# Optimization experiments

Hardware: AMD Instinct MI355X
Metric: run time of the kernel (lower is better)

The kernel has to match this reference:

```python
import jax, jax.numpy as jnp
import numpy as np

D = 256
H = 8
HD = D // H
LN_EPS = 1e-5


def setup_inputs() -> dict:
    key = jax.random.key(0)
    ks = jax.random.split(key, 20)
    N = 768
    s = lambda *sh: 1.0 / np.sqrt(sh[-1])
    inp = {
        "features": jax.random.normal(ks[0], (N, D), jnp.float32),
        "boxes": jax.random.uniform(ks[1], (N, 4), jnp.float32),
        # MultiheadAttention params (torch layout: [out, in])
        "in_proj_w": jax.random.normal(ks[2], (3 * D, D), jnp.float32) * s(D),
        "in_proj_b": jnp.zeros((3 * D,), jnp.float32),
        "out_proj_w": jax.random.normal(ks[3], (D, D), jnp.float32) * s(D),
        "out_proj_b": jnp.zeros((D,), jnp.float32),
        # similarity_net params
        "w1": jax.random.normal(ks[4], (256, 3 * D + 3), jnp.float32) * s(3 * D + 3),
        "b1": jnp.zeros((256,), jnp.float32),
        "ln_g": jnp.ones((256,), jnp.float32),
        "ln_b": jnp.zeros((256,), jnp.float32),
        "w2": jax.random.normal(ks[5], (128, 256), jnp.float32) * s(256),
        "b2": jnp.zeros((128,), jnp.float32),
        "w3": jax.random.normal(ks[6], (64, 128), jnp.float32) * s(128),
        "b3": jnp.zeros((64,), jnp.float32),
        "w4": jax.random.normal(ks[7], (32, 64), jnp.float32) * s(64),
        "b4": jnp.zeros((32,), jnp.float32),
        "w5": jax.random.normal(ks[8], (1, 32), jnp.float32) * s(32),
        "b5": jnp.zeros((1,), jnp.float32),
    }
    return inp


def _mha(x, in_w, in_b, out_w, out_b):
    # x: [N, D]; torch nn.MultiheadAttention self-attention (eval mode)
    N = x.shape[0]
    qkv = x @ in_w.T + in_b                      # [N, 3D]
    q, k, v = jnp.split(qkv, 3, axis=-1)
    q = q.reshape(N, H, HD).transpose(1, 0, 2)   # [H, N, HD]
    k = k.reshape(N, H, HD).transpose(1, 0, 2)
    v = v.reshape(N, H, HD).transpose(1, 0, 2)
    scores = jnp.einsum("hnd,hmd->hnm", q, k) / np.sqrt(HD)
    attn = jax.nn.softmax(scores, axis=-1)
    o = jnp.einsum("hnm,hmd->hnd", attn, v)      # [H, N, HD]
    o = o.transpose(1, 0, 2).reshape(N, D)
    return o @ out_w.T + out_b


def reference(features, boxes, in_proj_w, in_proj_b, out_proj_w, out_proj_b,
              w1, b1, ln_g, ln_b, w2, b2, w3, b3, w4, b4, w5, b5):
    N = features.shape[0]
    att = _mha(features, in_proj_w, in_proj_b, out_proj_w, out_proj_b)  # [N, D]

    fi = jnp.broadcast_to(att[:, None, :], (N, N, D))
    fj = jnp.broadcast_to(att[None, :, :], (N, N, D))
    bi = boxes[:, None, :]
    bj = boxes[None, :, :]
    x_dist = jnp.abs(bi[:, :, 0] - bj[:, :, 0])
    y_diff = bi[:, :, 1] - bj[:, :, 1]
    spatial = jnp.stack([x_dist, jnp.abs(y_diff), y_diff], axis=-1)    # [N, N, 3]
    pairs = jnp.concatenate([fi, fj, fi * fj, spatial], axis=-1)       # [N, N, 3D+3]

    h = jax.nn.relu(pairs @ w1.T + b1)
    mu = jnp.mean(h, axis=-1, keepdims=True)
    var = jnp.var(h, axis=-1, keepdims=True)
    h = (h - mu) / jnp.sqrt(var + LN_EPS) * ln_g + ln_b
    h = jax.nn.relu(h @ w2.T + b2)
    h = jax.nn.relu(h @ w3.T + b3)
    h = jax.nn.relu(h @ w4.T + b4)
    logits = (h @ w5.T + b5)[..., 0]                                   # [N, N]

    eye = jnp.eye(N, dtype=logits.dtype)
    return logits * (1.0 - eye) - 1e9 * eye
```

## Files before the change

kernel.cpp:

```cpp
#include <hip/hip_runtime.h>


typedef __attribute__((ext_vector_type(8))) __bf16 bf16x8;
typedef __attribute__((ext_vector_type(4))) float f32x4;
typedef __attribute__((ext_vector_type(8))) int i32x8;

__device__ __forceinline__ float bf2f(unsigned short u) {
    return __uint_as_float(((unsigned int)u) << 16);
}
__device__ __forceinline__ unsigned short f2bf(float f) {
    union { __bf16 b; unsigned short u; } cv;
    cv.b = (__bf16)f;
    return cv.u;
}
__device__ __forceinline__ unsigned pk2(float lo, float hi) {
    return (unsigned)f2bf(lo) | ((unsigned)f2bf(hi) << 16);
}
__device__ __forceinline__ int pk4_fp8(float a, float b, float c, float d) {
    int w = __builtin_amdgcn_cvt_pk_fp8_f32(a, b, 0, false);
    w = __builtin_amdgcn_cvt_pk_fp8_f32(c, d, w, true);
    return w;
}
__device__ __forceinline__ unsigned char f2fp8(float v) {
    return (unsigned char)(__builtin_amdgcn_cvt_pk_fp8_f32(v, 0.f, 0, false) & 0xff);
}
__device__ __forceinline__ bf16x8 load8f_bf(const float* p) {
    float4 a = *reinterpret_cast<const float4*>(p);
    float4 b = *reinterpret_cast<const float4*>(p + 4);
    union { bf16x8 v; unsigned u[4]; } cv;
    cv.u[0] = pk2(a.x, a.y); cv.u[1] = pk2(a.z, a.w);
    cv.u[2] = pk2(b.x, b.y); cv.u[3] = pk2(b.z, b.w);
    return cv.v;
}
#define SC1 0x7F7F7F7F
#define MFMA_MX(a, b, c) __builtin_amdgcn_mfma_scale_f32_16x16x128_f8f6f4( \
        (a), (b), (c), 0, 0, 0, SC1, 0, SC1)

__global__ __launch_bounds__(256) void pack_all(
    const float* __restrict__ features, const float* __restrict__ in_proj_w,
    const float* __restrict__ in_proj_b, const float* __restrict__ out_proj_w,
    const float* __restrict__ w1, const float* __restrict__ w2,
    const float* __restrict__ w3, const float* __restrict__ w4,
    const float* __restrict__ b1, const float* __restrict__ ln_g,
    const float* __restrict__ ln_b, const float* __restrict__ b2,
    const float* __restrict__ out_proj_b,
    unsigned short* __restrict__ qkvb, unsigned short* __restrict__ Vt,
    unsigned short* __restrict__ WcatB,
    unsigned char* __restrict__ w1c_mx, unsigned char* __restrict__ w1t_f8,
    unsigned char* __restrict__ w2g_mx, unsigned char* __restrict__ w3_mx,
    unsigned char* __restrict__ w4_f8,
    float* __restrict__ bias768, float* __restrict__ c1, float* __restrict__ c2)
{
    const int blk = blockIdx.x;
    if (blk < 716) {
        int t = blk * 256 + threadIdx.x;
        if (t < 65536) {
            WcatB[t] = f2bf(out_proj_w[t]);
        } else if (t < 131072) {
            int u = t - 65536;
            int e = u & 31, lane = (u >> 5) & 63, f = u >> 11;
            int mt = f & 15, ks = f >> 4;
            int o = mt * 16 + (lane & 15);
            int k = ks * 128 + ((lane >> 4) & 3) * 32 + e;
            w1c_mx[u] = f2fp8(w1[o * 771 + 512 + k]);
        } else if (t < 139264) {
            int u = t - 131072;
            int e = u & 7, lane = (u >> 3) & 63, f = u >> 9;
            int o = f * 16 + (lane & 15);
            int k = ((lane >> 4) & 3) * 8 + e;
            float v = (k < 3) ? w1[o * 771 + 768 + k] : 0.f;
            w1t_f8[u] = f2fp8(v);
        } else if (t < 172032) {
            int u = t - 139264;
            int e = u & 31, lane = (u >> 5) & 63, f = u >> 11;
            int mt = f & 7, ks = f >> 3;
            int p = mt * 16 + (lane & 15);
            int k = ks * 128 + ((lane >> 4) & 3) * 32 + e;
            w2g_mx[u] = f2fp8(w2[p * 256 + k] * ln_g[k]);
        } else if (t < 180224) {
            int u = t - 172032;
            int e = u & 31, lane = (u >> 5) & 63, f = u >> 11;
            int o = f * 16 + (lane & 15);
            int k = ((lane >> 4) & 3) * 32 + e;
            w3_mx[u] = f2fp8(w3[o * 128 + k]);
        } else if (t < 182272) {
            int u = t - 180224;
            int e = u & 7, lane = (u >> 3) & 63, f = u >> 9;
            int l15 = lane & 15, quad = lane >> 4;
            int ct = f & 1, kc = f >> 1;
            int o = ct * 16 + l15, k = kc * 32 + quad * 8 + e;
            w4_f8[u] = f2fp8(w4[o * 64 + k]);
        } else if (t < 183040) {
            int n = t - 182272;
            if (n < 256) bias768[n] = out_proj_b[n];
            else {
                int m = n - 256;
                float s = 0.f;
                for (int d = 0; d < 256; d += 4) {
                    float4 ob = *reinterpret_cast<const float4*>(&out_proj_b[d]);
                    const float* wr = (m < 256) ? &w1[m * 771 + d]
                                                : &w1[(m - 256) * 771 + 256 + d];
                    float4 w = *reinterpret_cast<const float4*>(wr);
                    s += ob.x * w.x + ob.y * w.y + ob.z * w.z + ob.w * w.w;
                }
                bias768[n] = s + ((m < 256) ? b1[m] : 0.f);
            }
        } else if (t < 183168) {
            int p = t - 183040;
            float s2 = 0.f, s1 = 0.f;
            for (int k = 0; k < 256; k += 4) {
                float4 w = *reinterpret_cast<const float4*>(&w2[p * 256 + k]);
                float4 g = *reinterpret_cast<const float4*>(&ln_g[k]);
                float4 lb = *reinterpret_cast<const float4*>(&ln_b[k]);
                s2 += g.x * w.x + g.y * w.y + g.z * w.z + g.w * w.w;
                s1 += lb.x * w.x + lb.y * w.y + lb.z * w.z + lb.w * w.w;
            }
            c2[p] = s2;
            c1[p] = s1 + b2[p];
        }
    } else if (blk < 1228) {
        const int n = blk - 716, e = threadIdx.x;
        const float* wrow = (n < 256) ? &w1[n * 771] : &w1[(n - 256) * 771 + 256];
        float acc = 0.f;
        for (int d = 0; d < 256; d += 4) {
            float4 w = *reinterpret_cast<const float4*>(&wrow[d]);
            acc += w.x * out_proj_w[(d + 0) * 256 + e];
            acc += w.y * out_proj_w[(d + 1) * 256 + e];
            acc += w.z * out_proj_w[(d + 2) * 256 + e];
            acc += w.w * out_proj_w[(d + 3) * 256 + e];
        }
        WcatB[(256 + n) * 256 + e] = f2bf(acc);
    } else {
        const int q = blk - 1228;
        const int bm = q % 12, bn = q / 12;
        const int wv = threadIdx.x >> 6, lane = threadIdx.x & 63;
        const int l15 = lane & 15, quad = lane >> 4;
        const int row0 = bm * 64 + wv * 16;
        const int col0 = bn * 64;
        f32x4 acc[4] = {};
        for (int kc = 0; kc < 8; ++kc) {
            bf16x8 a = load8f_bf(&features[(row0 + l15) * 256 + kc * 32 + quad * 8]);
#pragma unroll
            for (int ct = 0; ct < 4; ++ct) {
                bf16x8 b = load8f_bf(&in_proj_w[(col0 + ct * 16 + l15) * 256 + kc * 32 + quad * 8]);
                acc[ct] = __builtin_amdgcn_mfma_f32_16x16x32_bf16(a, b, acc[ct], 0, 0, 0);
            }
        }
#pragma unroll
        for (int ct = 0; ct < 4; ++ct)
#pragma unroll
            for (int r = 0; r < 4; ++r) {
                int row = row0 + quad * 4 + r, col = col0 + ct * 16 + l15;
                float v = acc[ct][r] + in_proj_b[col];
                if (col < 512) qkvb[row * 768 + col] = f2bf(v);
                else           Vt[(col - 512) * 768 + row] = f2bf(v);
            }
    }
}

__global__ __launch_bounds__(256) void gemm_attab(
    const unsigned short* __restrict__ A, const unsigned short* __restrict__ W,
    const float* __restrict__ bias, float* __restrict__ att,
    float* __restrict__ AB)
{
    const int wv = threadIdx.x >> 6, lane = threadIdx.x & 63;
    const int l15 = lane & 15, quad = lane >> 4;
    const int row0 = blockIdx.x * 64 + wv * 16;
    const int col0 = blockIdx.y * 64;
    f32x4 acc[4] = {};
    for (int kc = 0; kc < 8; ++kc) {
        bf16x8 a = *reinterpret_cast<const bf16x8*>(&A[(row0 + l15) * 256 + kc * 32 + quad * 8]);
#pragma unroll
        for (int ct = 0; ct < 4; ++ct) {
            bf16x8 b = *reinterpret_cast<const bf16x8*>(&W[(col0 + ct * 16 + l15) * 256 + kc * 32 + quad * 8]);
            acc[ct] = __builtin_amdgcn_mfma_f32_16x16x32_bf16(a, b, acc[ct], 0, 0, 0);
        }
    }
#pragma unroll
    for (int ct = 0; ct < 4; ++ct)
#pragma unroll
        for (int r = 0; r < 4; ++r) {
            int row = row0 + quad * 4 + r, col = col0 + ct * 16 + l15;
            float v = acc[ct][r] + bias[col];
            if (col < 256) att[row * 256 + col] = v;
            else           AB[row * 512 + (col - 256)] = v;
        }
}

#define SP 776

__global__ __launch_bounds__(256) void attn_mfma(
    const unsigned short* __restrict__ qkvb, const unsigned short* __restrict__ Vt,
    unsigned short* __restrict__ Obf)
{
    __shared__ __align__(16) unsigned short smS[32 * SP];
    __shared__ float s_inv[32];
    const int h = blockIdx.x, q0 = blockIdx.y * 32, hb = h * 32;
    const int tid = threadIdx.x, wave = tid >> 6, lane = tid & 63;
    const int l15 = lane & 15, quad = lane >> 4;

    bf16x8 af[2];
#pragma unroll
    for (int mt = 0; mt < 2; ++mt)
        af[mt] = *reinterpret_cast<const bf16x8*>(&qkvb[(q0 + mt * 16 + l15) * 768 + hb + quad * 8]);
#pragma unroll
    for (int ct = 0; ct < 12; ++ct) {
        int n0 = wave * 192 + ct * 16;
        bf16x8 b = *reinterpret_cast<const bf16x8*>(&qkvb[(n0 + l15) * 768 + 256 + hb + quad * 8]);
#pragma unroll
        for (int mt = 0; mt < 2; ++mt) {
            f32x4 c = {};
            c = __builtin_amdgcn_mfma_f32_16x16x32_bf16(af[mt], b, c, 0, 0, 0);
#pragma unroll
            for (int r = 0; r < 4; ++r)
                smS[(mt * 16 + quad * 4 + r) * SP + n0 + l15] =
                    f2bf(c[r] * 0.17677669529663689f);
        }
    }
    __syncthreads();

    {
        const int row = tid >> 3, part = tid & 7;
        unsigned short* rp = &smS[row * SP + part * 96];
        float ls = 0.f;
#pragma unroll
        for (int c8 = 0; c8 < 12; ++c8) {
            uint4 v = *reinterpret_cast<const uint4*>(&rp[c8 * 8]);
            const unsigned short* pe = reinterpret_cast<const unsigned short*>(&v);
            unsigned short o8[8];
#pragma unroll
            for (int e = 0; e < 8; ++e) {
                float ev = __expf(bf2f(pe[e]));
                ls += ev;
                o8[e] = f2bf(ev);
            }
            *reinterpret_cast<uint4*>(&rp[c8 * 8]) = *reinterpret_cast<const uint4*>(o8);
        }
        ls += __shfl_xor(ls, 1, 64);
        ls += __shfl_xor(ls, 2, 64);
        ls += __shfl_xor(ls, 4, 64);
        if (part == 0) s_inv[row] = 1.0f / ls;
    }
    __syncthreads();

    const int row0 = (wave >> 1) * 16, cg = wave & 1;
    f32x4 accp = {};
    for (int kc = 0; kc < 24; ++kc) {
        bf16x8 a = *reinterpret_cast<const bf16x8*>(&smS[(row0 + l15) * SP + kc * 32 + quad * 8]);
        bf16x8 b = *reinterpret_cast<const bf16x8*>(&Vt[(hb + cg * 16 + l15) * 768 + kc * 32 + quad * 8]);
        accp = __builtin_amdgcn_mfma_f32_16x16x32_bf16(a, b, accp, 0, 0, 0);
    }
#pragma unroll
    for (int r = 0; r < 4; ++r) {
        int rloc = row0 + quad * 4 + r;
        Obf[(q0 + rloc) * 256 + hb + cg * 16 + l15] = f2bf(accp[r] * s_inv[rloc]);
    }
}

__global__ __launch_bounds__(512, 2) void pair_mlp(
    const float* __restrict__ att, const float* __restrict__ AB,
    const unsigned char* __restrict__ w1c_mx, const unsigned char* __restrict__ w1t_f8,
    const unsigned char* __restrict__ w2g_mx, const unsigned char* __restrict__ w3_mx,
    const unsigned char* __restrict__ w4_f8,
    const float* __restrict__ boxes,
    const float* __restrict__ c1, const float* __restrict__ c2,
    const float* __restrict__ b3, const float* __restrict__ b4,
    const float* __restrict__ w5, const float* __restrict__ b5,
    float* __restrict__ out)
{
    __shared__ __align__(16) unsigned char smH[64 * 384];
    __shared__ __align__(16) unsigned char smH1[64 * 256];
    __shared__ __align__(16) unsigned char smH2[64 * 192];
    __shared__ __align__(16) unsigned char smH3[64 * 72];
    __shared__ float s_psum[64][8], s_pssq[64][8];
    __shared__ float s_mu[64], s_rs[64];
    __shared__ float s_l5[64][2];

    const int i    = blockIdx.x;
    const int j0   = blockIdx.y * 64;
    const int tid  = threadIdx.x;
    const int wave = tid >> 6;
    const int lane = tid & 63;
    const int l15  = lane & 15;
    const int quad = lane >> 4;

    {
        const int g = tid & 63;
        const int ch = g >> 2;
        float4 fi4 = *reinterpret_cast<const float4*>(&att[i * 256 + g * 4]);
#pragma unroll 4
        for (int it = 0; it < 8; ++it) {
            int r = (tid >> 6) + it * 8;
            float4 aj = *reinterpret_cast<const float4*>(&att[(j0 + r) * 256 + g * 4]);
            int cs = ch ^ (r & 15);
            *reinterpret_cast<int*>(&smH[r * 384 + cs * 16 + (g & 3) * 4]) =
                pk4_fp8(aj.x * fi4.x, aj.y * fi4.y, aj.z * fi4.z, aj.w * fi4.w);
        }
    }
    if (tid < 64) {
        int j = j0 + tid;
        float xd = fabsf(boxes[i * 4 + 0] - boxes[j * 4 + 0]);
        float yd = boxes[i * 4 + 1] - boxes[j * 4 + 1];
        unsigned char* tb = &smH[tid * 384 + 256 + (tid & 3) * 24];
        *reinterpret_cast<int*>(tb)      = pk4_fp8(xd, fabsf(yd), yd, 0.f);
        *reinterpret_cast<int*>(tb + 4)  = 0;
        *reinterpret_cast<long long*>(tb + 8)  = 0;
        *reinterpret_cast<long long*>(tb + 16) = 0;
        *reinterpret_cast<long long*>(tb + 24) = 0;
    }
    __syncthreads();

    f32x4 acc1[2][4] = {};
#pragma unroll
    for (int ks = 0; ks < 2; ++ks) {
        i32x8 a0 = *reinterpret_cast<const i32x8*>(&w1c_mx[((ks * 16 + wave * 2 + 0) * 64 + lane) * 32]);
        i32x8 a1 = *reinterpret_cast<const i32x8*>(&w1c_mx[((ks * 16 + wave * 2 + 1) * 64 + lane) * 32]);
        const int cb = ks * 8 + quad * 2;
#pragma unroll
        for (int nt = 0; nt < 4; ++nt) {
            const unsigned char* rp = &smH[(nt * 16 + l15) * 384];
            union { i32x8 v; uint4 q[2]; } b;
            b.q[0] = *reinterpret_cast<const uint4*>(rp + ((cb    ) ^ l15) * 16);
            b.q[1] = *reinterpret_cast<const uint4*>(rp + ((cb + 1) ^ l15) * 16);
            acc1[0][nt] = MFMA_MX(a0, b.v, acc1[0][nt]);
            acc1[1][nt] = MFMA_MX(a1, b.v, acc1[1][nt]);
        }
    }
    {
        long long a0 = *reinterpret_cast<const long long*>(&w1t_f8[((wave * 2 + 0) * 64 + lane) * 8]);
        long long a1 = *reinterpret_cast<const long long*>(&w1t_f8[((wave * 2 + 1) * 64 + lane) * 8]);
#pragma unroll
        for (int nt = 0; nt < 4; ++nt) {
            long long b = *reinterpret_cast<const long long*>(
                &smH[(nt * 16 + l15) * 384 + 256 + (l15 & 3) * 24 + quad * 8]);
            acc1[0][nt] = __builtin_amdgcn_mfma_f32_16x16x32_fp8_fp8(a0, b, acc1[0][nt], 0, 0, 0);
            acc1[1][nt] = __builtin_amdgcn_mfma_f32_16x16x32_fp8_fp8(a1, b, acc1[1][nt], 0, 0, 0);
        }
    }

    const int o0 = wave * 32;
    float vsum[4] = {}, vssq[4] = {};
#pragma unroll
    for (int mt = 0; mt < 2; ++mt) {
        int o = o0 + mt * 16 + quad * 4;
        float4 Ai = *reinterpret_cast<const float4*>(&AB[i * 512 + o]);
        float AiA[4] = {Ai.x, Ai.y, Ai.z, Ai.w};
#pragma unroll
        for (int nt = 0; nt < 4; ++nt) {
            int j = nt * 16 + l15;
            float4 Bj = *reinterpret_cast<const float4*>(&AB[(j0 + j) * 512 + 256 + o]);
            float BjA[4] = {Bj.x, Bj.y, Bj.z, Bj.w};
#pragma unroll
            for (int r = 0; r < 4; ++r) {
                float v = fmaxf(acc1[mt][nt][r] + AiA[r] + BjA[r], 0.f);
                acc1[mt][nt][r] = v;
                vsum[nt] += v; vssq[nt] += v * v;
            }
        }
    }
#pragma unroll
    for (int nt = 0; nt < 4; ++nt) {
        vsum[nt] += __shfl_xor(vsum[nt], 16, 64);
        vsum[nt] += __shfl_xor(vsum[nt], 32, 64);
        vssq[nt] += __shfl_xor(vssq[nt], 16, 64);
        vssq[nt] += __shfl_xor(vssq[nt], 32, 64);
    }
    if (quad == 0)
#pragma unroll
        for (int nt = 0; nt < 4; ++nt) {
            s_psum[nt * 16 + l15][wave] = vsum[nt];
            s_pssq[nt * 16 + l15][wave] = vssq[nt];
        }
#pragma unroll
    for (int mt = 0; mt < 2; ++mt) {
        const int ch = wave * 2 + mt;
#pragma unroll
        for (int nt = 0; nt < 4; ++nt) {
            int j = nt * 16 + l15;
            *reinterpret_cast<int*>(&smH1[j * 256 + (ch ^ l15) * 16 + quad * 4]) =
                pk4_fp8(acc1[mt][nt][0], acc1[mt][nt][1], acc1[mt][nt][2], acc1[mt][nt][3]);
        }
    }
    __syncthreads();
    if (wave == 0) {
        int j = lane;
        float sm = 0.f, sq = 0.f;
#pragma unroll
        for (int w = 0; w < 8; ++w) { sm += s_psum[j][w]; sq += s_pssq[j][w]; }
        sm *= (1.0f / 256.0f); sq *= (1.0f / 256.0f);
        s_mu[j] = sm;
        s_rs[j] = rsqrtf(sq - sm * sm + 1e-5f);
    }

    f32x4 acc2[4] = {};
#pragma unroll
    for (int ks = 0; ks < 2; ++ks) {
        i32x8 a = *reinterpret_cast<const i32x8*>(&w2g_mx[((ks * 8 + wave) * 64 + lane) * 32]);
        const int cb = ks * 8 + quad * 2;
#pragma unroll
        for (int nt = 0; nt < 4; ++nt) {
            const unsigned char* rp = &smH1[(nt * 16 + l15) * 256];
            union { i32x8 v; uint4 q[2]; } b;
            b.q[0] = *reinterpret_cast<const uint4*>(rp + ((cb    ) ^ l15) * 16);
            b.q[1] = *reinterpret_cast<const uint4*>(rp + ((cb + 1) ^ l15) * 16);
            acc2[nt] = MFMA_MX(a, b.v, acc2[nt]);
        }
    }
    __syncthreads();
    {
        int p = wave * 16 + quad * 4;
        float4 C1 = *reinterpret_cast<const float4*>(&c1[p]);
        float4 C2 = *reinterpret_cast<const float4*>(&c2[p]);
        float C1A[4] = {C1.x, C1.y, C1.z, C1.w};
        float C2A[4] = {C2.x, C2.y, C2.z, C2.w};
#pragma unroll
        for (int nt = 0; nt < 4; ++nt) {
            int j = nt * 16 + l15;
            float mu = s_mu[j], rs = s_rs[j];
            float vv[4];
#pragma unroll
            for (int r = 0; r < 4; ++r)
                vv[r] = fmaxf(rs * (acc2[nt][r] - mu * C2A[r]) + C1A[r], 0.f);
            *reinterpret_cast<int*>(&smH2[j * 192 + (wave ^ (l15 & 7)) * 16 + quad * 4]) =
                pk4_fp8(vv[0], vv[1], vv[2], vv[3]);
        }
    }
    __syncthreads();

    const int qt  = wave >> 1;
    const int jh2 = wave & 1;
    f32x4 acc3[2] = {};
    {
        i32x8 a = *reinterpret_cast<const i32x8*>(&w3_mx[(qt * 64 + lane) * 32]);
        const int cb = quad * 2;
#pragma unroll
        for (int ntl = 0; ntl < 2; ++ntl) {
            int j = (jh2 * 2 + ntl) * 16 + l15;
            const unsigned char* rp = &smH2[j * 192];
            union { i32x8 v; uint4 q[2]; } b;
            b.q[0] = *reinterpret_cast<const uint4*>(rp + ((cb    ) ^ (l15 & 7)) * 16);
            b.q[1] = *reinterpret_cast<const uint4*>(rp + ((cb + 1) ^ (l15 & 7)) * 16);
            acc3[ntl] = MFMA_MX(a, b.v, acc3[ntl]);
        }
    }
    {
        int q = qt * 16 + quad * 4;
        float4 B3 = *reinterpret_cast<const float4*>(&b3[q]);
        float B3A[4] = {B3.x, B3.y, B3.z, B3.w};
#pragma unroll
        for (int ntl = 0; ntl < 2; ++ntl) {
            int j = (jh2 * 2 + ntl) * 16 + l15;
            float vv[4];
#pragma unroll
            for (int r = 0; r < 4; ++r)
                vv[r] = fmaxf(acc3[ntl][r] + B3A[r], 0.f);
            *reinterpret_cast<int*>(&smH3[j * 72 + q]) = pk4_fp8(vv[0], vv[1], vv[2], vv[3]);
        }
    }
    __syncthreads();

    const int mt4 = wave & 1;
    const int jq  = wave >> 1;
    f32x4 acc4 = {};
#pragma unroll
    for (int kc = 0; kc < 2; ++kc) {
        long long a = *reinterpret_cast<const long long*>(&w4_f8[((kc * 2 + mt4) * 64 + lane) * 8]);
        int j = jq * 16 + l15;
        long long b = *reinterpret_cast<const long long*>(&smH3[j * 72 + kc * 32 + quad * 8]);
        acc4 = __builtin_amdgcn_mfma_f32_16x16x32_fp8_fp8(a, b, acc4, 0, 0, 0);
    }
    {
        int o4 = mt4 * 16 + quad * 4;
        float4 B4 = *reinterpret_cast<const float4*>(&b4[o4]);
        float4 W5 = *reinterpret_cast<const float4*>(&w5[o4]);
        float B4A[4] = {B4.x, B4.y, B4.z, B4.w};
        float W5A[4] = {W5.x, W5.y, W5.z, W5.w};
        float part = 0.f;
#pragma unroll
        for (int r = 0; r < 4; ++r)
            part += fmaxf(acc4[r] + B4A[r], 0.f) * W5A[r];
        part += __shfl_xor(part, 16, 64);
        part += __shfl_xor(part, 32, 64);
        if (quad == 0)
            s_l5[jq * 16 + l15][mt4] = part;
    }
    __syncthreads();
    if (tid < 64) {
        int j = j0 + tid;
        float v = s_l5[tid][0] + s_l5[tid][1] + b5[0];
        out[i * 768 + j] = (j == i) ? -1.0e9f : v;
    }
}

extern "C" void kernel_launch(void* const* d_in, const int* in_sizes, int n_in,
                              void* d_out, int out_size, void* d_ws, size_t ws_size,
                              hipStream_t stream)
{
    const float* features   = (const float*)d_in[0];
    const float* boxes      = (const float*)d_in[1];
    const float* in_proj_w  = (const float*)d_in[2];
    const float* in_proj_b  = (const float*)d_in[3];
    const float* out_proj_w = (const float*)d_in[4];
    const float* out_proj_b = (const float*)d_in[5];
    const float* w1  = (const float*)d_in[6];
    const float* b1  = (const float*)d_in[7];
    const float* ln_g = (const float*)d_in[8];
    const float* ln_b = (const float*)d_in[9];
    const float* w2  = (const float*)d_in[10];
    const float* b2  = (const float*)d_in[11];
    const float* w3  = (const float*)d_in[12];
    const float* b3  = (const float*)d_in[13];
    const float* w4  = (const float*)d_in[14];
    const float* b4  = (const float*)d_in[15];
    const float* w5  = (const float*)d_in[16];
    const float* b5  = (const float*)d_in[17];
    float* out = (float*)d_out;

    char* p = (char*)d_ws;
    unsigned short* qkvb  = (unsigned short*)p; p += 768 * 768 * 2;
    unsigned short* Vt    = (unsigned short*)p; p += 256 * 768 * 2;
    unsigned short* Obf   = (unsigned short*)p; p += 768 * 256 * 2;
    unsigned short* WcatB = (unsigned short*)p; p += 196608 * 2;
    float* att = (float*)p; p += 768 * 256 * 4;
    float* AB  = (float*)p; p += 768 * 512 * 4;
    unsigned char* w1c_mx = (unsigned char*)p; p += 65536;
    unsigned char* w1t_f8 = (unsigned char*)p; p += 8192;
    unsigned char* w2g_mx = (unsigned char*)p; p += 32768;
    unsigned char* w3_mx  = (unsigned char*)p; p += 8192;
    unsigned char* w4_f8  = (unsigned char*)p; p += 2048;
    float* bias768 = (float*)p; p += 768 * 4;
    float* c1v     = (float*)p; p += 128 * 4;
    float* c2v     = (float*)p; p += 128 * 4;

    pack_all<<<dim3(1372), dim3(256), 0, stream>>>(features, in_proj_w,
        in_proj_b, out_proj_w, w1, w2, w3, w4, b1, ln_g, ln_b, b2, out_proj_b,
        qkvb, Vt, WcatB, w1c_mx, w1t_f8, w2g_mx, w3_mx, w4_f8,
        bias768, c1v, c2v);
    attn_mfma<<<dim3(8, 24), dim3(256), 0, stream>>>(qkvb, Vt, Obf);
    gemm_attab<<<dim3(12, 12), dim3(256), 0, stream>>>(Obf, WcatB, bias768,
        att, AB);
    pair_mlp<<<dim3(768, 12), dim3(512), 0, stream>>>(att, AB,
        w1c_mx, w1t_f8, w2g_mx, w3_mx, w4_f8, boxes, c1v, c2v,
        b3, b4, w5, b5, out);
}
```

Before: 283.3 us.

## Split QKV GEMM out and co-schedule attention with weight packing in one launch

The QKV projection moves into its own small kernel. Attention blocks are merged with the weight-packing and W1·out_proj fold blocks into a single launch, so packing work runs alongside attention instead of alongside the QKV GEMM. This lets the independent packing overlap the attention phase and keeps the kernel count unchanged. The cost is that every block in the merged kernel now reserves the attention shared-memory footprint, which may lower occupancy for the packing blocks.

```diff
diff --git a/kernel.cpp b/kernel.cpp
--- a/kernel.cpp
+++ b/kernel.cpp
@@ -36,24 +36,133 @@
 #define MFMA_MX(a, b, c) __builtin_amdgcn_mfma_scale_f32_16x16x128_f8f6f4( \
         (a), (b), (c), 0, 0, 0, SC1, 0, SC1)
 
-__global__ __launch_bounds__(256) void pack_all(
+__global__ __launch_bounds__(256) void qkv_gemm(
     const float* __restrict__ features, const float* __restrict__ in_proj_w,
-    const float* __restrict__ in_proj_b, const float* __restrict__ out_proj_w,
-    const float* __restrict__ w1, const float* __restrict__ w2,
-    const float* __restrict__ w3, const float* __restrict__ w4,
-    const float* __restrict__ b1, const float* __restrict__ ln_g,
-    const float* __restrict__ ln_b, const float* __restrict__ b2,
-    const float* __restrict__ out_proj_b,
-    unsigned short* __restrict__ qkvb, unsigned short* __restrict__ Vt,
+    const float* __restrict__ in_proj_b,
+    unsigned short* __restrict__ qkvb, unsigned short* __restrict__ Vt)
+{
+    const int q = blockIdx.x;
+    const int bm = q % 12, bn = q / 12;
+    const int wv = threadIdx.x >> 6, lane = threadIdx.x & 63;
+    const int l15 = lane & 15, quad = lane >> 4;
+    const int row0 = bm * 64 + wv * 16;
+    const int col0 = bn * 64;
+    f32x4 acc[4] = {};
+    for (int kc = 0; kc < 8; ++kc) {
+        bf16x8 a = load8f_bf(&features[(row0 + l15) * 256 + kc * 32 + quad * 8]);
+#pragma unroll
+        for (int ct = 0; ct < 4; ++ct) {
+            bf16x8 b = load8f_bf(&in_proj_w[(col0 + ct * 16 + l15) * 256 + kc * 32 + quad * 8]);
+            acc[ct] = __builtin_amdgcn_mfma_f32_16x16x32_bf16(a, b, acc[ct], 0, 0, 0);
+        }
+    }
+#pragma unroll
+    for (int ct = 0; ct < 4; ++ct)
+#pragma unroll
+        for (int r = 0; r < 4; ++r) {
+            int row = row0 + quad * 4 + r, col = col0 + ct * 16 + l15;
+            float v = acc[ct][r] + in_proj_b[col];
+            if (col < 512) qkvb[row * 768 + col] = f2bf(v);
+            else           Vt[(col - 512) * 768 + row] = f2bf(v);
+        }
+}
+
+#define SP 776
+
+__global__ __launch_bounds__(256) void attn_pack(
+    const unsigned short* __restrict__ qkvb, const unsigned short* __restrict__ Vt,
+    unsigned short* __restrict__ Obf,
+    const float* __restrict__ out_proj_w, const float* __restrict__ w1,
+    const float* __restrict__ w2, const float* __restrict__ w3,
+    const float* __restrict__ w4, const float* __restrict__ b1,
+    const float* __restrict__ ln_g, const float* __restrict__ ln_b,
+    const float* __restrict__ b2, const float* __restrict__ out_proj_b,
     unsigned short* __restrict__ WcatB,
     unsigned char* __restrict__ w1c_mx, unsigned char* __restrict__ w1t_f8,
     unsigned char* __restrict__ w2g_mx, unsigned char* __restrict__ w3_mx,
     unsigned char* __restrict__ w4_f8,
     float* __restrict__ bias768, float* __restrict__ c1, float* __restrict__ c2)
 {
+    __shared__ __align__(16) unsigned short smS[32 * SP];
+    __shared__ float s_inv[32];
     const int blk = blockIdx.x;
-    if (blk < 716) {
-        int t = blk * 256 + threadIdx.x;
+    const int tid = threadIdx.x;
+
+    if (blk < 192) {
+        const int h = blk & 7, q0 = (blk >> 3) * 32, hb = h * 32;
+        const int wave = tid >> 6, lane = tid & 63;
+        const int l15 = lane & 15, quad = lane >> 4;
+
+        bf16x8 af[2];
+#pragma unroll
+        for (int mt = 0; mt < 2; ++mt)
+            af[mt] = *reinterpret_cast<const bf16x8*>(&qkvb[(q0 + mt * 16 + l15) * 768 + hb + quad * 8]);
+#pragma unroll
+        for (int ct = 0; ct < 12; ++ct) {
+            int n0 = wave * 192 + ct * 16;
+            bf16x8 b = *reinterpret_cast<const bf16x8*>(&qkvb[(n0 + l15) * 768 + 256 + hb + quad * 8]);
+#pragma unroll
+            for (int mt = 0; mt < 2; ++mt) {
+                f32x4 c = {};
+                c = __builtin_amdgcn_mfma_f32_16x16x32_bf16(af[mt], b, c, 0, 0, 0);
+#pragma unroll
+                for (int r = 0; r < 4; ++r)
+                    smS[(mt * 16 + quad * 4 + r) * SP + n0 + l15] =
+                        f2bf(c[r] * 0.17677669529663689f);
+            }
+        }
+        __syncthreads();
+
+        {
+            const int row = tid >> 3, part = tid & 7;
+            unsigned short* rp = &smS[row * SP + part * 96];
+            float ls = 0.f;
+#pragma unroll
+            for (int c8 = 0; c8 < 12; ++c8) {
+                uint4 v = *reinterpret_cast<const uint4*>(&rp[c8 * 8]);
+                const unsigned short* pe = reinterpret_cast<const unsigned short*>(&v);
+                unsigned short o8[8];
+#pragma unroll
+                for (int e = 0; e < 8; ++e) {
+                    float ev = __expf(bf2f(pe[e]));
+                    ls += ev;
+                    o8[e] = f2bf(ev);
+                }
+                *reinterpret_cast<uint4*>(&rp[c8 * 8]) = *reinterpret_cast<const uint4*>(o8);
+            }
+            ls += __shfl_xor(ls, 1, 64);
+            ls += __shfl_xor(ls, 2, 64);
+            ls += __shfl_xor(ls, 4, 64);
+            if (part == 0) s_inv[row] = 1.0f / ls;
+        }
+        __syncthreads();
+
+        const int row0 = (wave >> 1) * 16, cg = wave & 1;
+        f32x4 accp = {};
+        for (int kc = 0; kc < 24; ++kc) {
+            bf16x8 a = *reinterpret_cast<const bf16x8*>(&smS[(row0 + l15) * SP + kc * 32 + quad * 8]);
+            bf16x8 b = *reinterpret_cast<const bf16x8*>(&Vt[(hb + cg * 16 + l15) * 768 + kc * 32 + quad * 8]);
+            accp = __builtin_amdgcn_mfma_f32_16x16x32_bf16(a, b, accp, 0, 0, 0);
+        }
+#pragma unroll
+        for (int r = 0; r < 4; ++r) {
+            int rloc = row0 + quad * 4 + r;
+            Obf[(q0 + rloc) * 256 + hb + cg * 16 + l15] = f2bf(accp[r] * s_inv[rloc]);
+        }
+    } else if (blk < 704) {
+        const int n = blk - 192, e = tid;
+        const float* wrow = (n < 256) ? &w1[n * 771] : &w1[(n - 256) * 771 + 256];
+        float acc = 0.f;
+        for (int d = 0; d < 256; d += 4) {
+            float4 w = *reinterpret_cast<const float4*>(&wrow[d]);
+            acc += w.x * out_proj_w[(d + 0) * 256 + e];
+            acc += w.y * out_proj_w[(d + 1) * 256 + e];
+            acc += w.z * out_proj_w[(d + 2) * 256 + e];
+            acc += w.w * out_proj_w[(d + 3) * 256 + e];
+        }
+        WcatB[(256 + n) * 256 + e] = f2bf(acc);
+    } else {
+        int t = (blk - 704) * 256 + tid;
         if (t < 65536) {
             WcatB[t] = f2bf(out_proj_w[t]);
         } else if (t < 131072) {
@@ -118,43 +227,6 @@
             c2[p] = s2;
             c1[p] = s1 + b2[p];
         }
-    } else if (blk < 1228) {
-        const int n = blk - 716, e = threadIdx.x;
-        const float* wrow = (n < 256) ? &w1[n * 771] : &w1[(n - 256) * 771 + 256];
-        float acc = 0.f;
-        for (int d = 0; d < 256; d += 4) {
-            float4 w = *reinterpret_cast<const float4*>(&wrow[d]);
-            acc += w.x * out_proj_w[(d + 0) * 256 + e];
-            acc += w.y * out_proj_w[(d + 1) * 256 + e];
-            acc += w.z * out_proj_w[(d + 2) * 256 + e];
-            acc += w.w * out_proj_w[(d + 3) * 256 + e];
-        }
-        WcatB[(256 + n) * 256 + e] = f2bf(acc);
-    } else {
-        const int q = blk - 1228;
-        const int bm = q % 12, bn = q / 12;
-        const int wv = threadIdx.x >> 6, lane = threadIdx.x & 63;
-        const int l15 = lane & 15, quad = lane >> 4;
-        const int row0 = bm * 64 + wv * 16;
-        const int col0 = bn * 64;
-        f32x4 acc[4] = {};
-        for (int kc = 0; kc < 8; ++kc) {
-            bf16x8 a = load8f_bf(&features[(row0 + l15) * 256 + kc * 32 + quad * 8]);
-#pragma unroll
-            for (int ct = 0; ct < 4; ++ct) {
-                bf16x8 b = load8f_bf(&in_proj_w[(col0 + ct * 16 + l15) * 256 + kc * 32 + quad * 8]);
-                acc[ct] = __builtin_amdgcn_mfma_f32_16x16x32_bf16(a, b, acc[ct], 0, 0, 0);
-            }
-        }
-#pragma unroll
-        for (int ct = 0; ct < 4; ++ct)
-#pragma unroll
-            for (int r = 0; r < 4; ++r) {
-                int row = row0 + quad * 4 + r, col = col0 + ct * 16 + l15;
-                float v = acc[ct][r] + in_proj_b[col];
-                if (col < 512) qkvb[row * 768 + col] = f2bf(v);
-                else           Vt[(col - 512) * 768 + row] = f2bf(v);
-            }
     }
 }
 
@@ -185,76 +257,6 @@
             if (col < 256) att[row * 256 + col] = v;
             else           AB[row * 512 + (col - 256)] = v;
         }
-}
-
-#define SP 776
-
-__global__ __launch_bounds__(256) void attn_mfma(
-    const unsigned short* __restrict__ qkvb, const unsigned short* __restrict__ Vt,
-    unsigned short* __restrict__ Obf)
-{
-    __shared__ __align__(16) unsigned short smS[32 * SP];
-    __shared__ float s_inv[32];
-    const int h = blockIdx.x, q0 = blockIdx.y * 32, hb = h * 32;
-    const int tid = threadIdx.x, wave = tid >> 6, lane = tid & 63;
-    const int l15 = lane & 15, quad = lane >> 4;
-
-    bf16x8 af[2];
-#pragma unroll
-    for (int mt = 0; mt < 2; ++mt)
-        af[mt] = *reinterpret_cast<const bf16x8*>(&qkvb[(q0 + mt * 16 + l15) * 768 + hb + quad * 8]);
-#pragma unroll
-    for (int ct = 0; ct < 12; ++ct) {
-        int n0 = wave * 192 + ct * 16;
-        bf16x8 b = *reinterpret_cast<const bf16x8*>(&qkvb[(n0 + l15) * 768 + 256 + hb + quad * 8]);
-#pragma unroll
-        for (int mt = 0; mt < 2; ++mt) {
-            f32x4 c = {};
-            c = __builtin_amdgcn_mfma_f32_16x16x32_bf16(af[mt], b, c, 0, 0, 0);
-#pragma unroll
-            for (int r = 0; r < 4; ++r)
-                smS[(mt * 16 + quad * 4 + r) * SP + n0 + l15] =
-                    f2bf(c[r] * 0.17677669529663689f);
-        }
-    }
-    __syncthreads();
-
-    {
-        const int row = tid >> 3, part = tid & 7;
-        unsigned short* rp = &smS[row * SP + part * 96];
-        float ls = 0.f;
-#pragma unroll
-        for (int c8 = 0; c8 < 12; ++c8) {
-            uint4 v = *reinterpret_cast<const uint4*>(&rp[c8 * 8]);
-            const unsigned short* pe = reinterpret_cast<const unsigned short*>(&v);
-            unsigned short o8[8];
-#pragma unroll
-            for (int e = 0; e < 8; ++e) {
-                float ev = __expf(bf2f(pe[e]));
-                ls += ev;
-                o8[e] = f2bf(ev);
-            }
-            *reinterpret_cast<uint4*>(&rp[c8 * 8]) = *reinterpret_cast<const uint4*>(o8);
-        }
-        ls += __shfl_xor(ls, 1, 64);
-        ls += __shfl_xor(ls, 2, 64);
-        ls += __shfl_xor(ls, 4, 64);
-        if (part == 0) s_inv[row] = 1.0f / ls;
-    }
-    __syncthreads();
-
-    const int row0 = (wave >> 1) * 16, cg = wave & 1;
-    f32x4 accp = {};
-    for (int kc = 0; kc < 24; ++kc) {
-        bf16x8 a = *reinterpret_cast<const bf16x8*>(&smS[(row0 + l15) * SP + kc * 32 + quad * 8]);
-        bf16x8 b = *reinterpret_cast<const bf16x8*>(&Vt[(hb + cg * 16 + l15) * 768 + kc * 32 + quad * 8]);
-        accp = __builtin_amdgcn_mfma_f32_16x16x32_bf16(a, b, accp, 0, 0, 0);
-    }
-#pragma unroll
-    for (int r = 0; r < 4; ++r) {
-        int rloc = row0 + quad * 4 + r;
-        Obf[(q0 + rloc) * 256 + hb + cg * 16 + l15] = f2bf(accp[r] * s_inv[rloc]);
-    }
 }
 
 __global__ __launch_bounds__(512, 2) void pair_mlp(
@@ -532,11 +534,11 @@
     float* c1v     = (float*)p; p += 128 * 4;
     float* c2v     = (float*)p; p += 128 * 4;
 
-    pack_all<<<dim3(1372), dim3(256), 0, stream>>>(features, in_proj_w,
-        in_proj_b, out_proj_w, w1, w2, w3, w4, b1, ln_g, ln_b, b2, out_proj_b,
-        qkvb, Vt, WcatB, w1c_mx, w1t_f8, w2g_mx, w3_mx, w4_f8,
-        bias768, c1v, c2v);
-    attn_mfma<<<dim3(8, 24), dim3(256), 0, stream>>>(qkvb, Vt, Obf);
+    qkv_gemm<<<dim3(144), dim3(256), 0, stream>>>(features, in_proj_w,
+        in_proj_b, qkvb, Vt);
+    attn_pack<<<dim3(1420), dim3(256), 0, stream>>>(qkvb, Vt, Obf,
+        out_proj_w, w1, w2, w3, w4, b1, ln_g, ln_b, b2, out_proj_b,
+        WcatB, w1c_mx, w1t_f8, w2g_mx, w3_mx, w4_f8, bias768, c1v, c2v);
     gemm_attab<<<dim3(12, 12), dim3(256), 0, stream>>>(Obf, WcatB, bias768,
         att, AB);
     pair_mlp<<<dim3(768, 12), dim3(512), 0, stream>>>(att, AB,
```

New measurement: 284.8 us. About the same (+0.5%).
